# Kernel tuning notes

Measured on AMD Instinct MI355X. Metric: run time of the kernel, lower is better.

## Reference

```python
import jax, jax.numpy as jnp
import numpy as np

K = 121          # kernel_size
C = 3            # channels
PAD = (K - 1) // 2  # 60, replicate padding so output matches input spatial size


def setup_inputs() -> dict:
    key = jax.random.key(0)
    k1, k2 = jax.random.split(key)
    x = jax.random.normal(k1, (8, C, 512, 512), dtype=jnp.float32)
    sigma = jax.random.uniform(k2, (), dtype=jnp.float32)
    return {"x": x, "sigma": sigma}


def _gaussian_kernel(sigma):
    # sigma -> sigma*8 + 16, variance = sigma**2 (as in torch forward)
    s = sigma * 8.0 + 16.0
    variance = s * s
    coord = jnp.arange(K, dtype=jnp.float32) - (K - 1) / 2.0  # centered coords
    diff = -(coord[:, None] ** 2 + coord[None, :] ** 2)       # [K,K], -((x-m)^2+(y-m)^2)
    kern = jnp.exp(diff / (2.0 * variance))
    # the 1/(2*pi*variance) prefactor cancels under normalization
    kern = kern / jnp.sum(kern)
    return kern


def reference(x, sigma):
    kern = _gaussian_kernel(sigma)
    # depthwise weights: [out_ch=C, in_ch/groups=1, K, K]
    w = jnp.broadcast_to(kern[None, None, :, :], (C, 1, K, K))
    # replicate padding (torch 'replicate' == jnp 'edge')
    xp = jnp.pad(x, ((0, 0), (0, 0), (PAD, PAD), (PAD, PAD)), mode="edge")
    out = jax.lax.conv_general_dilated(
        xp, w,
        window_strides=(1, 1),
        padding="VALID",
        dimension_numbers=("NCHW", "OIHW", "NCHW"),
        feature_group_count=C,
    )
    return out
```

## Files before the change

### kernel.cpp

```cpp
#include <hip/hip_runtime.h>


#define HH      512
#define WW      512
#define PLANE   (512 * 512)
#define NIMG    24
#define HPG_ROW 972

__device__ __forceinline__ void make_weights(const float* __restrict__ sigma,
                                             float* __restrict__ wlds, int tid) {
    const float s = sigma[0] * 8.0f + 16.0f;
    const float inv2v = 1.0f / (2.0f * s * s);
    float sum = 0.0f;
    #pragma unroll
    for (int k = 0; k <= 120; ++k) {
        const float c = (float)k - 60.0f;
        sum += __expf(-c * c * inv2v);
    }
    if (tid < 128) {
        float g = 0.0f;
        if (tid < 121) {
            const float c = (float)tid - 60.0f;
            g = __expf(-c * c * inv2v);
        }
        wlds[tid] = g / sum;
    }
}

#define V_OCT(CUR, NXT, KO)                                               \
    { *(float4*)&wq[0] = *(const float4*)&wlds[(KO) * 8];                 \
      *(float4*)&wq[4] = *(const float4*)&wlds[(KO) * 8 + 4];             \
      _Pragma("unroll")                                                   \
      for (int ki = 0; ki < 8; ++ki) {                                    \
          int rr = r0 - 52 + (KO) * 8 + ki;                               \
          rr = rr < 0 ? 0 : (rr > HH - 1 ? HH - 1 : rr);                  \
          NXT[ki] = *(const float2*)&src[(size_t)rr * WW];                \
          const float wk = wq[ki];                                        \
          _Pragma("unroll")                                               \
          for (int j = 0; j < 8; ++j) {                                   \
              const int idx = ki + j;                                     \
              const float2 v = (idx < 8) ? CUR[idx] : NXT[idx - 8];       \
              vac[j].x += wk * v.x; vac[j].y += wk * v.y;                 \
          }                                                               \
      }                                                                   \
    }

#define LOADG(DST, G)                                                     \
    { *(float4*)&DST[0] = *(const float4*)&bs[(G) * 12];                  \
      *(float4*)&DST[4] = *(const float4*)&bs[(G) * 12 + 4]; }

#define H_OCT(W0, W1, W2, W3, KO)                                         \
    { LOADG(W3, (KO) + 3)                                                 \
      *(float4*)&wq[0] = *(const float4*)&wlds[(KO) * 8];                 \
      *(float4*)&wq[4] = *(const float4*)&wlds[(KO) * 8 + 4];             \
      _Pragma("unroll")                                                   \
      for (int ki = 0; ki < 8; ++ki) {                                    \
          const float wk = wq[ki];                                        \
          _Pragma("unroll")                                               \
          for (int j = 0; j < 16; ++j) {                                  \
              const int idx = ki + j;                                     \
              const float v = (idx < 8) ? W0[idx]                         \
                            : (idx < 16) ? W1[idx - 8] : W2[idx - 16];    \
              acc[j] += wk * v;                                           \
          }                                                               \
      }                                                                   \
    }

__global__ __launch_bounds__(256, 4) void blur_fused(
        const float* __restrict__ x, const float* __restrict__ sigma,
        float* __restrict__ out) {
    __shared__ float sm[8 * HPG_ROW];
    __shared__ float wlds[128];
    const int tid = threadIdx.x;
    const int r0  = blockIdx.x * 8;
    const int c0  = tid * 2;
    const float* __restrict__ src = x + (size_t)blockIdx.y * PLANE + c0;

    float2 wa[8], wb[8], vac[8];
    float  wq[8];
    #pragma unroll
    for (int m = 0; m < 8; ++m) {
        int rr = r0 - 60 + m;
        rr = rr < 0 ? 0 : rr;
        wa[m] = *(const float2*)&src[(size_t)rr * WW];
    }
    make_weights(sigma, wlds, tid);
    #pragma unroll
    for (int j = 0; j < 8; ++j) vac[j] = make_float2(0.f, 0.f);
    __syncthreads();

    #pragma unroll 1
    for (int ko = 0; ko < 16; ko += 2) {
        V_OCT(wa, wb, ko)
        V_OCT(wb, wa, ko + 1)
    }

    {
        const int p  = c0 + 60;
        const int la = (p >> 3) * 12 + (p & 7);
        #pragma unroll
        for (int j = 0; j < 8; ++j)
            *(float2*)&sm[j * HPG_ROW + la] = vac[j];
    }
    __syncthreads();

    if (tid < 136) {
        const int p    = (tid < 60) ? tid : 512 + tid;
        const int dsta = (p >> 3) * 12 + (p & 7);
        const int srca = (tid < 60) ? (7 * 12 + 4)
                                    : (71 * 12 + 3);
        #pragma unroll
        for (int r = 0; r < 8; ++r)
            sm[r * HPG_ROW + dsta] = sm[r * HPG_ROW + srca];
    }
    __syncthreads();

    const int r = tid >> 5;
    const int L = tid & 31;
    const float* __restrict__ bs = sm + r * HPG_ROW + L * 24;

    float w0[8], w1[8], w2[8], w3[8];
    float acc[16];
    #pragma unroll
    for (int j = 0; j < 16; ++j) acc[j] = 0.0f;

    LOADG(w0, 0)
    LOADG(w1, 1)
    LOADG(w2, 2)

    #pragma unroll 1
    for (int ko = 0; ko < 16; ko += 4) {
        H_OCT(w0, w1, w2, w3, ko)
        H_OCT(w1, w2, w3, w0, ko + 1)
        H_OCT(w2, w3, w0, w1, ko + 2)
        H_OCT(w3, w0, w1, w2, ko + 3)
    }

    float* __restrict__ dst = out + (size_t)blockIdx.y * PLANE
                                  + (size_t)(r0 + r) * WW + L * 16;
    *(float4*)(dst)      = make_float4(acc[0],  acc[1],  acc[2],  acc[3]);
    *(float4*)(dst + 4)  = make_float4(acc[4],  acc[5],  acc[6],  acc[7]);
    *(float4*)(dst + 8)  = make_float4(acc[8],  acc[9],  acc[10], acc[11]);
    *(float4*)(dst + 12) = make_float4(acc[12], acc[13], acc[14], acc[15]);
}

extern "C" void kernel_launch(void* const* d_in, const int* in_sizes, int n_in,
                              void* d_out, int out_size, void* d_ws, size_t ws_size,
                              hipStream_t stream) {
    const float* x     = (const float*)d_in[0];
    const float* sigma = (const float*)d_in[1];
    float* out = (float*)d_out;
    blur_fused<<<dim3(HH / 8, NIMG), dim3(256), 0, stream>>>(x, sigma, out);
}
```

Measured before the change: 130.1 us.

## Split horizontal pass into two interleaved 8-wide strips and swizzle block order

Each thread in the horizontal pass now computes two 8-column output strips 256 columns apart instead of one contiguous 16-column strip. Adjacent lanes therefore read adjacent 12-float groups in LDS, which should cut bank conflicts, and the LDS row pitch grows to 984 with the extra groups zero-padded. Block indices are also remapped so that consecutive launched blocks spread across planes and row tiles, which may improve cache locality or load balance across the XCDs. The cost is more register arrays in flight, which could raise register pressure.

New measurement: 117.9 us. -9.4%, faster.

```diff
diff --git a/kernel.cpp b/kernel.cpp
--- a/kernel.cpp
+++ b/kernel.cpp
@@ -5,7 +5,7 @@
 #define WW      512
 #define PLANE   (512 * 512)
 #define NIMG    24
-#define HPG_ROW 972
+#define HPG_ROW 984
 
 __device__ __forceinline__ void make_weights(const float* __restrict__ sigma,
                                              float* __restrict__ wlds, int tid) {
@@ -49,19 +49,23 @@
     { *(float4*)&DST[0] = *(const float4*)&bs[(G) * 12];                  \
       *(float4*)&DST[4] = *(const float4*)&bs[(G) * 12 + 4]; }
 
-#define H_OCT(W0, W1, W2, W3, KO)                                         \
-    { LOADG(W3, (KO) + 3)                                                 \
+#define H_OCT2(A0, A1, A2, A3, B0, B1, B2, B3, KO)                        \
+    { LOADG(A3, L + (KO) + 3)                                             \
+      LOADG(B3, L + 32 + (KO) + 3)                                        \
       *(float4*)&wq[0] = *(const float4*)&wlds[(KO) * 8];                 \
       *(float4*)&wq[4] = *(const float4*)&wlds[(KO) * 8 + 4];             \
       _Pragma("unroll")                                                   \
       for (int ki = 0; ki < 8; ++ki) {                                    \
           const float wk = wq[ki];                                        \
           _Pragma("unroll")                                               \
-          for (int j = 0; j < 16; ++j) {                                  \
+          for (int j = 0; j < 8; ++j) {                                   \
               const int idx = ki + j;                                     \
-              const float v = (idx < 8) ? W0[idx]                         \
-                            : (idx < 16) ? W1[idx - 8] : W2[idx - 16];    \
-              acc[j] += wk * v;                                           \
+              const float vA = (idx < 8) ? A0[idx]                        \
+                             : (idx < 16) ? A1[idx - 8] : A2[idx - 16];   \
+              const float vB = (idx < 8) ? B0[idx]                        \
+                             : (idx < 16) ? B1[idx - 8] : B2[idx - 16];   \
+              accA[j] += wk * vA;                                         \
+              accB[j] += wk * vB;                                         \
           }                                                               \
       }                                                                   \
     }
@@ -72,9 +76,14 @@
     __shared__ float sm[8 * HPG_ROW];
     __shared__ float wlds[128];
     const int tid = threadIdx.x;
-    const int r0  = blockIdx.x * 8;
-    const int c0  = tid * 2;
-    const float* __restrict__ src = x + (size_t)blockIdx.y * PLANE + c0;
+
+    const int lid   = blockIdx.x + gridDim.x * blockIdx.y;
+    const int tile  = (lid & 7) * 192 + (lid >> 3);
+    const int r0    = (tile & 63) * 8;
+    const int plane = tile >> 6;
+
+    const int c0 = tid * 2;
+    const float* __restrict__ src = x + (size_t)plane * PLANE + c0;
 
     float2 wa[8], wb[8], vac[8];
     float  wq[8];
@@ -104,44 +113,47 @@
     }
     __syncthreads();
 
-    if (tid < 136) {
-        const int p    = (tid < 60) ? tid : 512 + tid;
+    if (tid < 144) {
+        int p, srca;
+        if (tid < 60)       { p = tid;       srca = 7 * 12 + 4;  }
+        else if (tid < 136) { p = 512 + tid; srca = 71 * 12 + 3; }
+        else                { p = 512 + tid; srca = -1;          }
         const int dsta = (p >> 3) * 12 + (p & 7);
-        const int srca = (tid < 60) ? (7 * 12 + 4)
-                                    : (71 * 12 + 3);
         #pragma unroll
         for (int r = 0; r < 8; ++r)
-            sm[r * HPG_ROW + dsta] = sm[r * HPG_ROW + srca];
+            sm[r * HPG_ROW + dsta] = (srca < 0) ? 0.0f
+                                                : sm[r * HPG_ROW + srca];
     }
     __syncthreads();
 
     const int r = tid >> 5;
     const int L = tid & 31;
-    const float* __restrict__ bs = sm + r * HPG_ROW + L * 24;
+    const float* __restrict__ bs = sm + r * HPG_ROW;
 
-    float w0[8], w1[8], w2[8], w3[8];
-    float acc[16];
+    float a0[8], a1[8], a2[8], a3[8];
+    float b0[8], b1[8], b2[8], b3[8];
+    float accA[8], accB[8];
     #pragma unroll
-    for (int j = 0; j < 16; ++j) acc[j] = 0.0f;
+    for (int j = 0; j < 8; ++j) { accA[j] = 0.0f; accB[j] = 0.0f; }
 
-    LOADG(w0, 0)
-    LOADG(w1, 1)
-    LOADG(w2, 2)
+    LOADG(a0, L)      LOADG(b0, L + 32)
+    LOADG(a1, L + 1)  LOADG(b1, L + 33)
+    LOADG(a2, L + 2)  LOADG(b2, L + 34)
 
     #pragma unroll 1
     for (int ko = 0; ko < 16; ko += 4) {
-        H_OCT(w0, w1, w2, w3, ko)
-        H_OCT(w1, w2, w3, w0, ko + 1)
-        H_OCT(w2, w3, w0, w1, ko + 2)
-        H_OCT(w3, w0, w1, w2, ko + 3)
+        H_OCT2(a0, a1, a2, a3, b0, b1, b2, b3, ko)
+        H_OCT2(a1, a2, a3, a0, b1, b2, b3, b0, ko + 1)
+        H_OCT2(a2, a3, a0, a1, b2, b3, b0, b1, ko + 2)
+        H_OCT2(a3, a0, a1, a2, b3, b0, b1, b2, ko + 3)
     }
 
-    float* __restrict__ dst = out + (size_t)blockIdx.y * PLANE
-                                  + (size_t)(r0 + r) * WW + L * 16;
-    *(float4*)(dst)      = make_float4(acc[0],  acc[1],  acc[2],  acc[3]);
-    *(float4*)(dst + 4)  = make_float4(acc[4],  acc[5],  acc[6],  acc[7]);
-    *(float4*)(dst + 8)  = make_float4(acc[8],  acc[9],  acc[10], acc[11]);
-    *(float4*)(dst + 12) = make_float4(acc[12], acc[13], acc[14], acc[15]);
+    float* __restrict__ dst = out + (size_t)plane * PLANE
+                                  + (size_t)(r0 + r) * WW + L * 8;
+    *(float4*)(dst)        = make_float4(accA[0], accA[1], accA[2], accA[3]);
+    *(float4*)(dst + 4)    = make_float4(accA[4], accA[5], accA[6], accA[7]);
+    *(float4*)(dst + 256)  = make_float4(accB[0], accB[1], accB[2], accB[3]);
+    *(float4*)(dst + 260)  = make_float4(accB[4], accB[5], accB[6], accB[7]);
 }
 
 extern "C" void kernel_launch(void* const* d_in, const int* in_sizes, int n_in,
```
